# Kernel tuning notes

Measured on AMD Instinct MI355X. Metric: run time of the kernel, lower is better.

Reference implementation:

```python
import jax, jax.numpy as jnp
import numpy as np

B, N, H, NH, DEPTH = 4, 128, 512, 8, 4
HD = H // NH
TN = B * N
MH = int(H * 4.0)
EHD = 64
SCALE = HD ** -0.5

def _ln(x):
    m = jnp.mean(x, axis=-1, keepdims=True)
    v = jnp.mean(jnp.square(x - m), axis=-1, keepdims=True)
    return (x - m) * jax.lax.rsqrt(v + 1e-6)

def _gelu(x):
    return jax.nn.gelu(x, approximate=True)

def setup_inputs():
    rng = np.random.RandomState(0)
    topo_np = (rng.rand(B, N, N) < 0.15).astype(np.float32)
    sym = (topo_np + topo_np.transpose(0, 2, 1)) > 0
    b, i, j = np.nonzero(sym)  # same lexicographic order as torch nonzero
    edge_index = np.stack([i + b * N, j + b * N]).astype(np.int32)
    ks = jax.random.split(jax.random.key(0), 16)
    def w(k, shape, fan_in):
        return jax.random.normal(k, shape, jnp.float32) / np.float32(np.sqrt(fan_in))
    z = lambda *s: jnp.zeros(s, jnp.float32)
    return {
        "topo": jnp.asarray(topo_np),
        "weight": jax.random.normal(ks[0], (B, N), jnp.float32),
        "edge_index": jnp.asarray(edge_index),
        "w_topo": w(ks[1], (N, H), N), "b_topo": z(H),
        "w_w": w(ks[2], (1, H), 1), "b_w": z(H),
        "n_emb": 0.02 * jax.random.normal(ks[3], (N, H), jnp.float32),
        "wq": w(ks[4], (DEPTH, H, H), H), "bq": z(DEPTH, H),
        "wk": w(ks[5], (DEPTH, H, H), H), "bk": z(DEPTH, H),
        "wv": w(ks[6], (DEPTH, H, H), H), "bv": z(DEPTH, H),
        "wo": w(ks[7], (DEPTH, H, H), H), "bo": z(DEPTH, H),
        "w1": w(ks[8], (DEPTH, H, MH), H), "b1": z(DEPTH, MH),
        "w2": w(ks[9], (DEPTH, MH, H), MH), "b2": z(DEPTH, H),
        "ew1": w(ks[10], (3 * H, EHD), 3 * H), "eb1": z(EHD),
        "ew2": w(ks[11], (EHD, EHD), EHD), "eb2": z(EHD),
        "ew3": w(ks[12], (EHD, 1), EHD), "eb3": z(1),
    }

def _forward(topo, weight, edge_index, w_topo, b_topo, w_w, b_w, n_emb,
             wq, bq, wk, bk, wv, bv, wo, bo, w1, b1, w2, b2,
             ew1, eb1, ew2, eb2, ew3, eb3):
    src, dst = edge_index[0], edge_index[1]
    tsym = topo + jnp.swapaxes(topo, 1, 2)                      # (B,N,N)
    t = jnp.einsum('bnm,mh->bnh', tsym, w_topo) + b_topo        # topo_emb
    l = weight[..., None] * w_w[0] + b_w                        # weight_emb: Linear(1,H)
    x = (t + l + n_emb[None]).reshape(TN, H)
    for d in range(DEPTH):
        h = _ln(x)
        Q = (h @ wq[d] + bq[d]).reshape(TN, NH, HD)
        K = (h @ wk[d] + bk[d]).reshape(TN, NH, HD)
        V = (h @ wv[d] + bv[d]).reshape(TN, NH, HD)
        s = jnp.einsum('ehd,ehd->eh', Q[dst], K[src]) * SCALE   # (E,NH) per-edge QK dot
        m = jnp.maximum(jax.ops.segment_max(s, dst, num_segments=TN), -1e9)
        e = jnp.exp(s - m[dst])
        zs = jax.ops.segment_sum(e, dst, num_segments=TN)
        aw = e / (zs[dst] + 1e-12)                              # scatter_softmax
        msg = aw[..., None] * V[src]                            # (E,NH,HD)
        agg = jax.ops.segment_sum(msg, dst, num_segments=TN).reshape(TN, H)
        x = agg @ wo[d] + bo[d] + x
        h = _ln(x)
        x = _gelu(h @ w1[d] + b1[d]) @ w2[d] + b2[d] + x
    xb = x.reshape(B, N, H)
    xi = jnp.broadcast_to(xb[:, :, None, :], (B, N, N, H))
    xj = jnp.broadcast_to(xb[:, None, :, :], (B, N, N, H))
    f = jnp.concatenate([xi, xj, xi * xj], axis=-1)             # (B,N,N,3H)
    g = _gelu(f @ ew1 + eb1)
    g = _gelu(g @ ew2 + eb2)
    p = jax.nn.sigmoid((g @ ew3 + eb3)[..., 0])
    p = 0.5 * (p + jnp.swapaxes(p, 1, 2))
    p = p * (1.0 - jnp.eye(N, dtype=p.dtype))                   # zero diagonal
    p = p * (tsym > 0).astype(p.dtype)                          # mask to existing edges
    return p

def reference(topo, weight, edge_index, w_topo, b_topo, w_w, b_w, n_emb,
              wq, bq, wk, bk, wv, bv, wo, bo, w1, b1, w2, b2,
              ew1, eb1, ew2, eb2, ew3, eb3):
    return _forward(topo, weight, edge_index, w_topo, b_topo, w_w, b_w, n_emb,
                    wq, bq, wk, bk, wv, bv, wo, bo, w1, b1, w2, b2,
                    ew1, eb1, ew2, eb2, ew3, eb3)
```

## Files before the change

kernel.cpp:

```cpp
#include <hip/hip_runtime.h>
#include <hip/hip_bf16.h>
#include <math.h>

typedef __attribute__((ext_vector_type(8))) _Float16 f16x8;
typedef __attribute__((ext_vector_type(8))) short short8;
typedef __attribute__((ext_vector_type(4))) float f32x4;
typedef unsigned short u16;

__device__ __forceinline__ float gelu_f(float x) {
    float x3 = x * x * x;
    return 0.5f * x * (1.0f + tanhf(0.7978845608028654f * (x + 0.044715f * x3)));
}
__device__ __forceinline__ u16 f2h(float v) {
    _Float16 h = (_Float16)v;
    return *(u16*)&h;
}
__device__ __forceinline__ float h2f(u16 u) {
    _Float16 h = *(_Float16*)&u;
    return (float)h;
}

__global__ __launch_bounds__(256) void x0row_k(const float* __restrict__ topo,
                                               const float* __restrict__ weight,
                                               const float* __restrict__ w_topo,
                                               const float* __restrict__ b_topo,
                                               const float* __restrict__ w_w,
                                               const float* __restrict__ b_w,
                                               const float* __restrict__ n_emb,
                                               float* __restrict__ tsym,
                                               float* __restrict__ x,
                                               u16* __restrict__ h16) {
    int bn = blockIdx.x;
    int b = bn >> 7, n = bn & 127;
    int tid = threadIdx.x;
    __shared__ float tsr[128];
    __shared__ float red[256];
    if (tid < 128) {
        float v = topo[bn * 128 + tid] + topo[(b << 14) + (tid << 7) + n];
        tsr[tid] = v;
        tsym[bn * 128 + tid] = v;
    }
    __syncthreads();
    int c0 = tid, c1 = tid + 256;
    float acc0 = 0.f, acc1 = 0.f;
#pragma unroll 4
    for (int m = 0; m < 128; ++m) {
        float t = tsr[m];
        acc0 += t * w_topo[m * 512 + c0];
        acc1 += t * w_topo[m * 512 + c1];
    }
    float wgt = weight[bn];
    float v0 = acc0 + b_topo[c0] + wgt * w_w[c0] + b_w[c0] + n_emb[n * 512 + c0];
    float v1 = acc1 + b_topo[c1] + wgt * w_w[c1] + b_w[c1] + n_emb[n * 512 + c1];
    x[bn * 512 + c0] = v0;
    x[bn * 512 + c1] = v1;
    red[tid] = v0 + v1;
    __syncthreads();
    for (int off = 128; off > 0; off >>= 1) { if (tid < off) red[tid] += red[tid + off]; __syncthreads(); }
    float mean = red[0] * (1.0f / 512.0f);
    __syncthreads();
    float d0 = v0 - mean, d1 = v1 - mean;
    red[tid] = d0 * d0 + d1 * d1;
    __syncthreads();
    for (int off = 128; off > 0; off >>= 1) { if (tid < off) red[tid] += red[tid + off]; __syncthreads(); }
    float rs = rsqrtf(red[0] * (1.0f / 512.0f) + 1e-6f);
    h16[bn * 512 + c0] = f2h(d0 * rs);
    h16[bn * 512 + c1] = f2h(d1 * rs);
}

__global__ __launch_bounds__(256) void prep_k(
    const float* __restrict__ wq, const float* __restrict__ wk, const float* __restrict__ wv,
    const float* __restrict__ wo, const float* __restrict__ w1, const float* __restrict__ w2,
    const float* __restrict__ ew1,
    u16* __restrict__ qkvt, u16* __restrict__ wot,
    u16* __restrict__ w1t, u16* __restrict__ w2t,
    u16* __restrict__ eabt, u16* __restrict__ ect) {
    __shared__ u16 Hs[64][68];
    int bid = blockIdx.x;
    int region, tr, KK;
    u16* dh;
    if (bid < 768)       { region = 0; tr = bid;        KK = 512;  dh = qkvt; }
    else if (bid < 1024) { region = 1; tr = bid - 768;  KK = 512;  dh = wot; }
    else if (bid < 2048) { region = 2; tr = bid - 1024; KK = 512;  dh = w1t; }
    else if (bid < 3072) { region = 3; tr = bid - 2048; KK = 2048; dh = w2t; }
    else if (bid < 3088) { region = 4; tr = bid - 3072; KK = 512;  dh = eabt; }
    else                 { region = 5; tr = bid - 3088; KK = 512;  dh = ect; }
    int ktiles = KK >> 6;
    int tn = tr / ktiles, tk = tr % ktiles;
    int k0 = tk * 64, n0g = tn * 64;
    int tid = threadIdx.x;
#pragma unroll
    for (int p = 0; p < 4; ++p) {
        int kk = p * 16 + (tid >> 4);
        int nn = (tid & 15) * 4;
        int kg = k0 + kk, ng = n0g + nn;
        const float* src;
        if (region == 0) {
            int d = ng / 1536; int nr = ng - d * 1536; int sel = nr >> 9; int nc = nr & 511;
            const float* w = sel == 0 ? wq : (sel == 1 ? wk : wv);
            src = w + ((size_t)(d * 512 + kg)) * 512 + nc;
        } else if (region == 1) {
            int d = ng >> 9; int nc = ng & 511;
            src = wo + ((size_t)(d * 512 + kg)) * 512 + nc;
        } else if (region == 2) {
            int d = ng >> 11; int nc = ng & 2047;
            src = w1 + ((size_t)(d * 512 + kg)) * 2048 + nc;
        } else if (region == 3) {
            int d = ng >> 9; int nc = ng & 511;
            src = w2 + ((size_t)(d * 2048 + kg)) * 512 + nc;
        } else if (region == 4) {
            src = (ng < 64) ? (ew1 + (size_t)kg * 64 + ng) : (ew1 + (size_t)(512 + kg) * 64 + (ng - 64));
        } else {
            src = ew1 + (size_t)(1024 + kg) * 64 + ng;
        }
        float4 v = *(const float4*)src;
        *(ushort4*)&Hs[kk][nn] = make_ushort4(f2h(v.x), f2h(v.y), f2h(v.z), f2h(v.w));
    }
    __syncthreads();
#pragma unroll
    for (int p = 0; p < 2; ++p) {
        int chunk = p * 256 + tid;
        int nl = chunk >> 3;
        int k8 = (chunk & 7) * 8;
        ushort4 ha, hb;
        ha.x = Hs[k8 + 0][nl]; ha.y = Hs[k8 + 1][nl]; ha.z = Hs[k8 + 2][nl]; ha.w = Hs[k8 + 3][nl];
        hb.x = Hs[k8 + 4][nl]; hb.y = Hs[k8 + 5][nl]; hb.z = Hs[k8 + 6][nl]; hb.w = Hs[k8 + 7][nl];
        size_t dst = (size_t)(n0g + nl) * KK + k0 + k8;
        *(ushort4*)(dh + dst) = ha; *(ushort4*)(dh + dst + 4) = hb;
    }
}

template <int KC, bool PARTIAL, bool GELU, bool RES, bool OUTF, bool OUTS, bool EBIAS>
__global__ __launch_bounds__(256) void gemm2(
    const u16* __restrict__ A16, const u16* __restrict__ W16,
    const float* __restrict__ bias, const float* __restrict__ Rres,
    float* __restrict__ C, u16* __restrict__ C16,
    float* __restrict__ part, int lda, int N) {
    __shared__ u16 sbuf[2][2][64][32];
    const int tid = threadIdx.x;
    const int l = tid & 63;
    const int w = tid >> 6;
    const int bn0 = blockIdx.x * 64;
    const int bm0 = blockIdx.y * 64;
    const int z = blockIdx.z;

    const u16* gp[2];
#pragma unroll
    for (int i = 0; i < 2; ++i) {
        int o = (i * 4 + w) * 1024 + l * 16;
        int mat = o >> 12;
        int r = (o >> 6) & 63;
        int slot = (o >> 4) & 3;
        int lslot = slot ^ ((r >> 1) & 3);
        int kel = lslot * 8;
        const u16* basep = mat == 0 ? (A16 + (size_t)(bm0 + r) * lda)
                                    : (W16 + (size_t)(bn0 + r) * lda);
        gp[i] = basep + kel + z * KC;
    }

    f32x4 acc[2][2] = {};
    constexpr int S = KC / 32;

    auto stage = [&](int buf, int ko) {
#pragma unroll
        for (int i = 0; i < 2; ++i) {
            __builtin_amdgcn_global_load_lds(
                (const __attribute__((address_space(1))) void*)(gp[i] + ko),
                (__attribute__((address_space(3))) void*)((char*)&sbuf[buf][0][0][0] + (i * 4 + w) * 1024),
                16, 0, 0);
        }
    };
    auto compute = [&](int buf) {
        f16x8 a[2], b[2];
        int l15 = l & 15, lsl = l >> 4;
        int rA0 = (w & 1) * 32 + l15;
        int rB0 = (w >> 1) * 32 + l15;
#pragma unroll
        for (int f = 0; f < 2; ++f) {
            int rA = rA0 + f * 16;
            int rB = rB0 + f * 16;
            a[f] = *(const f16x8*)&sbuf[buf][0][rA][(lsl ^ ((rA >> 1) & 3)) * 8];
            b[f] = *(const f16x8*)&sbuf[buf][1][rB][(lsl ^ ((rB >> 1) & 3)) * 8];
        }
#pragma unroll
        for (int fm = 0; fm < 2; ++fm)
#pragma unroll
            for (int fn = 0; fn < 2; ++fn)
                acc[fm][fn] = __builtin_amdgcn_mfma_f32_16x16x32_f16(a[fm], b[fn], acc[fm][fn], 0, 0, 0);
    };

    stage(0, 0);
    __syncthreads();
#pragma unroll
    for (int s = 0; s < S; ++s) {
        if (s + 1 < S) stage((s + 1) & 1, (s + 1) * 32);
        compute(s & 1);
        __syncthreads();
    }

    int rb = bm0 + (w & 1) * 32 + ((l >> 4)) * 4;
    int cb = bn0 + (w >> 1) * 32 + (l & 15);
#pragma unroll
    for (int fm = 0; fm < 2; ++fm)
#pragma unroll
        for (int fn = 0; fn < 2; ++fn) {
            int col = cb + fn * 16;
            float bv;
            if (PARTIAL) bv = 0.f;
            else if (EBIAS) bv = col < 64 ? bias[col] : 0.f;
            else bv = bias[col];
#pragma unroll
            for (int r = 0; r < 4; ++r) {
                int row = rb + fm * 16 + r;
                float v = acc[fm][fn][r] + bv;
                if (PARTIAL) {
                    part[(size_t)z * 512 * N + (size_t)row * N + col] = v;
                } else {
                    if (GELU) v = gelu_f(v);
                    if (RES) v += Rres[(size_t)row * N + col];
                    if (OUTF) C[(size_t)row * N + col] = v;
                    if (OUTS) C16[(size_t)row * N + col] = f2h(v);
                }
            }
        }
}

template <int NZ, bool DOLN, bool DOSPLITX>
__global__ __launch_bounds__(256) void redln_k(const float* __restrict__ part,
                                               const float* __restrict__ bias,
                                               float* __restrict__ x,
                                               u16* __restrict__ h16) {
    int row = blockIdx.x;
    int tid = threadIdx.x;
    int c0 = tid, c1 = tid + 256;
    float v0 = bias[c0], v1 = bias[c1];
#pragma unroll
    for (int z = 0; z < NZ; ++z) {
        v0 += part[(size_t)z * 262144 + row * 512 + c0];
        v1 += part[(size_t)z * 262144 + row * 512 + c1];
    }
    v0 += x[row * 512 + c0];
    v1 += x[row * 512 + c1];
    x[row * 512 + c0] = v0;
    x[row * 512 + c1] = v1;
    if (DOSPLITX) {
        h16[row * 512 + c0] = f2h(v0);
        h16[row * 512 + c1] = f2h(v1);
    }
    if (DOLN) {
        __shared__ float red[256];
        red[tid] = v0 + v1;
        __syncthreads();
        for (int off = 128; off > 0; off >>= 1) { if (tid < off) red[tid] += red[tid + off]; __syncthreads(); }
        float mean = red[0] * (1.0f / 512.0f);
        __syncthreads();
        float d0 = v0 - mean, d1 = v1 - mean;
        red[tid] = d0 * d0 + d1 * d1;
        __syncthreads();
        for (int off = 128; off > 0; off >>= 1) { if (tid < off) red[tid] += red[tid + off]; __syncthreads(); }
        float rs = rsqrtf(red[0] * (1.0f / 512.0f) + 1e-6f);
        h16[row * 512 + c0] = f2h(d0 * rs);
        h16[row * 512 + c1] = f2h(d1 * rs);
    }
}

__global__ __launch_bounds__(256) void redqkv_k(const float* __restrict__ part,
                                                const float* __restrict__ bq,
                                                const float* __restrict__ bk,
                                                const float* __restrict__ bv,
                                                u16* __restrict__ qkv16) {
    int row = blockIdx.x;
    int tid = threadIdx.x;
#pragma unroll
    for (int u = 0; u < 6; ++u) {
        int col = tid + u * 256;
        float bias = col < 512 ? bq[col] : (col < 1024 ? bk[col - 512] : bv[col - 1024]);
        float v = bias + part[(size_t)row * 1536 + col]
                + part[(size_t)786432 + row * 1536 + col];
        qkv16[(size_t)row * 1536 + col] = f2h(v);
    }
}

__global__ __launch_bounds__(256) void attn_k(const u16* __restrict__ qkv16,
                                              const float* __restrict__ tsym,
                                              u16* __restrict__ agg16) {
    int tt = blockIdx.x, hh = blockIdx.y, b = blockIdx.z;
    __shared__ __align__(16) float Ks[128 * 68];
    __shared__ __align__(16) float Vt[64 * 132];
    __shared__ __align__(16) float Ss[16 * 132];
    __shared__ __align__(16) float Qs[16][68];
    int tid = threadIdx.x;
    {
        int j = tid >> 1, c0 = (tid & 1) * 32;
        const u16* kr = qkv16 + (size_t)(b * 128 + j) * 1536 + 512 + hh * 64 + c0;
        const u16* vr = kr + 512;
#pragma unroll
        for (int c = 0; c < 32; c += 8) {
            f16x8 kv = *(const f16x8*)(kr + c);
            f16x8 vv = *(const f16x8*)(vr + c);
#pragma unroll
            for (int q = 0; q < 8; ++q) {
                Ks[j * 68 + c0 + c + q] = (float)kv[q];
                Vt[(c0 + c + q) * 132 + j] = (float)vv[q];
            }
        }
    }
    {
        int rid = tid >> 4, c4 = (tid & 15) * 4;
        int grow = b * 128 + tt * 16 + rid;
        const u16* q0 = qkv16 + (size_t)grow * 1536 + hh * 64 + c4;
        Qs[rid][c4 + 0] = h2f(q0[0]);
        Qs[rid][c4 + 1] = h2f(q0[1]);
        Qs[rid][c4 + 2] = h2f(q0[2]);
        Qs[rid][c4 + 3] = h2f(q0[3]);
    }
    __syncthreads();
    {
        int j = tid & 127, th = tid >> 7;
        float acc[8] = {0.f, 0.f, 0.f, 0.f, 0.f, 0.f, 0.f, 0.f};
        for (int d0 = 0; d0 < 64; d0 += 4) {
            float4 kv = *(const float4*)&Ks[j * 68 + d0];
#pragma unroll
            for (int r = 0; r < 8; ++r) {
                float4 qv = *(const float4*)&Qs[th * 8 + r][d0];
                acc[r] += qv.x * kv.x + qv.y * kv.y + qv.z * kv.z + qv.w * kv.w;
            }
        }
        const float* tsr = tsym + ((size_t)b << 14) + (size_t)(tt * 16 + th * 8) * 128 + j;
#pragma unroll
        for (int r = 0; r < 8; ++r) {
            int t = th * 8 + r;
            float sv = (tsr[r * 128] > 0.f) ? acc[r] * 0.125f : -INFINITY;
            Ss[t * 132 + j] = sv;
        }
    }
    __syncthreads();
    {
        int row = tid >> 4, l16 = tid & 15;
        float v[8]; float m = -INFINITY;
#pragma unroll
        for (int c = 0; c < 8; ++c) { v[c] = Ss[row * 132 + l16 + c * 16]; m = fmaxf(m, v[c]); }
#pragma unroll
        for (int off = 8; off; off >>= 1) m = fmaxf(m, __shfl_xor(m, off));
        float ssum = 0.f;
#pragma unroll
        for (int c = 0; c < 8; ++c) {
            float e = (v[c] == -INFINITY) ? 0.f : __expf(v[c] - m);
            v[c] = e; ssum += e;
        }
#pragma unroll
        for (int off = 8; off; off >>= 1) ssum += __shfl_xor(ssum, off);
        float inv = 1.0f / (ssum + 1e-12f);
#pragma unroll
        for (int c = 0; c < 8; ++c) Ss[row * 132 + l16 + c * 16] = v[c] * inv;
    }
    __syncthreads();
    {
        int d = tid & 63, tq = tid >> 6;
        float a0 = 0.f, a1 = 0.f, a2 = 0.f, a3 = 0.f;
        for (int j0 = 0; j0 < 128; j0 += 4) {
            float4 vv = *(const float4*)&Vt[d * 132 + j0];
            float4 s0 = *(const float4*)&Ss[(tq * 4 + 0) * 132 + j0];
            float4 s1 = *(const float4*)&Ss[(tq * 4 + 1) * 132 + j0];
            float4 s2 = *(const float4*)&Ss[(tq * 4 + 2) * 132 + j0];
            float4 s3 = *(const float4*)&Ss[(tq * 4 + 3) * 132 + j0];
            a0 += s0.x * vv.x + s0.y * vv.y + s0.z * vv.z + s0.w * vv.w;
            a1 += s1.x * vv.x + s1.y * vv.y + s1.z * vv.z + s1.w * vv.w;
            a2 += s2.x * vv.x + s2.y * vv.y + s2.z * vv.z + s2.w * vv.w;
            a3 += s3.x * vv.x + s3.y * vv.y + s3.z * vv.z + s3.w * vv.w;
        }
        float accv[4] = {a0, a1, a2, a3};
        int growbase = b * 128 + tt * 16;
#pragma unroll
        for (int i = 0; i < 4; ++i) {
            int t = tq * 4 + i;
            agg16[(size_t)(growbase + t) * 512 + hh * 64 + d] = f2h(accv[i]);
        }
    }
}

__global__ __launch_bounds__(256) void redae_k(const float* __restrict__ part,
                                               const float* __restrict__ eb1,
                                               float* __restrict__ aebe) {
    int idx = blockIdx.x * 256 + threadIdx.x;
    int col = idx & 127;
    float v = col < 64 ? eb1[col] : 0.0f;
#pragma unroll
    for (int z = 0; z < 4; ++z) v += part[(size_t)z * 65536 + idx];
    aebe[idx] = v;
}

__global__ __launch_bounds__(256) void cross_k(const float* __restrict__ x,
                                               const u16* __restrict__ ect,
                                               float* __restrict__ C3) {
    int i = blockIdx.x, b = blockIdx.y;
    __shared__ float xis[512];
    __shared__ u16 As[2][128][32];
    int tid = threadIdx.x;
    {
        const float* xip = x + (size_t)(b * 128 + i) * 512;
        xis[tid] = xip[tid];
        xis[tid + 256] = xip[tid + 256];
    }
    int r = tid >> 1, half = tid & 1, koff = half * 16;
    const float* xr = x + (size_t)(b * 128 + r) * 512 + koff;
    int sw_r = (r >> 1) & 3;
    int lane = tid & 63, w = tid >> 6;
    int m0 = (w & 1) * 64, n0 = (w >> 1) * 32;
    int l15 = lane & 15, lsl = lane >> 4, kf = lsl * 8;
    const u16* pB0 = ect + (size_t)(n0 + l15) * 512 + kf;
    const u16* pB1 = ect + (size_t)(n0 + 16 + l15) * 512 + kf;
    f32x4 acc[4][2] = {};

    auto stageA = [&](int buf, int kbase) {
        float4 v0 = *(const float4*)(xr + kbase);
        float4 v1 = *(const float4*)(xr + kbase + 4);
        float4 v2 = *(const float4*)(xr + kbase + 8);
        float4 v3 = *(const float4*)(xr + kbase + 12);
        float xv[16] = {v0.x, v0.y, v0.z, v0.w, v1.x, v1.y, v1.z, v1.w,
                        v2.x, v2.y, v2.z, v2.w, v3.x, v3.y, v3.z, v3.w};
        short8 h0, h1;
#pragma unroll
        for (int q = 0; q < 8; ++q)
            h0[q] = (short)f2h(xv[q] * xis[kbase + koff + q]);
#pragma unroll
        for (int q = 0; q < 8; ++q)
            h1[q] = (short)f2h(xv[8 + q] * xis[kbase + koff + 8 + q]);
        *(short8*)&As[buf][r][((2 * half + 0) ^ sw_r) * 8] = h0;
        *(short8*)&As[buf][r][((2 * half + 1) ^ sw_r) * 8] = h1;
    };
    auto computeC = [&](int buf, int kbase) {
        f16x8 b0 = *(const f16x8*)(pB0 + kbase);
        f16x8 b1 = *(const f16x8*)(pB1 + kbase);
#pragma unroll
        for (int mf = 0; mf < 4; ++mf) {
            int rA = m0 + mf * 16 + l15;
            f16x8 ah = *(const f16x8*)&As[buf][rA][(lsl ^ ((rA >> 1) & 3)) * 8];
            acc[mf][0] = __builtin_amdgcn_mfma_f32_16x16x32_f16(ah, b0, acc[mf][0], 0, 0, 0);
            acc[mf][1] = __builtin_amdgcn_mfma_f32_16x16x32_f16(ah, b1, acc[mf][1], 0, 0, 0);
        }
    };

    __syncthreads();
    stageA(0, 0);
    __syncthreads();
    for (int s = 0; s < 16; ++s) {
        if (s < 15) stageA((s + 1) & 1, (s + 1) * 32);
        computeC(s & 1, s * 32);
        __syncthreads();
    }

    float* outp = C3 + (size_t)(b * 128 + i) * 128 * 64;
#pragma unroll
    for (int mf = 0; mf < 4; ++mf)
#pragma unroll
        for (int nf = 0; nf < 2; ++nf)
#pragma unroll
            for (int q = 0; q < 4; ++q)
                outp[(size_t)(m0 + mf * 16 + lsl * 4 + q) * 64 + (n0 + nf * 16 + l15)] = acc[mf][nf][q];
}

__global__ __launch_bounds__(256) void efin_k(const int* __restrict__ ei, int E,
                                              const float* __restrict__ C3,
                                              const float* __restrict__ aebe,
                                              const float* __restrict__ ew2, const float* __restrict__ eb2,
                                              const float* __restrict__ ew3, const float* __restrict__ eb3,
                                              float* __restrict__ P) {
    __shared__ float G1[32][66];
    __shared__ float G2[32][66];
    __shared__ int s_src[32], s_dst[32];
    int tid = threadIdx.x;
    int e0 = blockIdx.x * 32;
    if (tid < 32) {
        int e = e0 + tid;
        s_src[tid] = e < E ? ei[e] : 0;
        s_dst[tid] = e < E ? ei[E + e] : 0;
    }
    __syncthreads();
    {
        int e = tid >> 3, c8 = (tid & 7) * 8;
        int s = s_src[e], d = s_dst[e];
        int bB = s >> 7, i2 = s & 127, j2 = d & 127;
        const float* c3 = C3 + ((size_t)(bB * 128 + i2) * 128 + j2) * 64 + c8;
        const float* ap = aebe + (size_t)s * 128 + c8;
        const float* bp = aebe + (size_t)d * 128 + 64 + c8;
#pragma unroll
        for (int q = 0; q < 8; ++q)
            G1[e][c8 + q] = gelu_f(c3[q] + ap[q] + bp[q]);
    }
    __syncthreads();
    {
        int col = tid & 63, eq = tid >> 6;
        float acc[8];
#pragma unroll
        for (int i = 0; i < 8; ++i) acc[i] = eb2[col];
        for (int m = 0; m < 64; ++m) {
            float wv = ew2[m * 64 + col];
#pragma unroll
            for (int i = 0; i < 8; ++i) acc[i] += G1[eq * 8 + i][m] * wv;
        }
#pragma unroll
        for (int i = 0; i < 8; ++i) G2[eq * 8 + i][col] = gelu_f(acc[i]);
    }
    __syncthreads();
    {
        int el2 = tid >> 3, c8 = (tid & 7) * 8;
        float p = 0.f;
#pragma unroll
        for (int i = 0; i < 8; ++i) p += G2[el2][c8 + i] * ew3[c8 + i];
        p += __shfl_xor(p, 1); p += __shfl_xor(p, 2); p += __shfl_xor(p, 4);
        if ((tid & 7) == 0 && e0 + el2 < E) {
            float logit = p + eb3[0];
            int s = s_src[el2], d2 = s_dst[el2];
            int bB = s >> 7, i2 = s & 127, j2 = d2 & 127;
            P[(bB << 14) + (i2 << 7) + j2] = 1.0f / (1.0f + expf(-logit));
        }
    }
}

__global__ __launch_bounds__(256) void final_k(const float* __restrict__ tsym,
                                               const float* __restrict__ P,
                                               float* __restrict__ out) {
    int idx = blockIdx.x * 256 + threadIdx.x;
    int b = idx >> 14, i = (idx >> 7) & 127, j = idx & 127;
    float o = 0.0f;
    if (i != j && tsym[idx] > 0.0f)
        o = 0.5f * (P[idx] + P[(b << 14) + (j << 7) + i]);
    out[idx] = o;
}

extern "C" void kernel_launch(void* const* d_in, const int* in_sizes, int n_in,
                              void* d_out, int out_size, void* d_ws, size_t ws_size,
                              hipStream_t stream) {
    const float* topo   = (const float*)d_in[0];
    const float* weight = (const float*)d_in[1];
    const int*   ei     = (const int*)d_in[2];
    const float* w_topo = (const float*)d_in[3];
    const float* b_topo = (const float*)d_in[4];
    const float* w_w    = (const float*)d_in[5];
    const float* b_w    = (const float*)d_in[6];
    const float* n_emb  = (const float*)d_in[7];
    const float* wq = (const float*)d_in[8];  const float* bq = (const float*)d_in[9];
    const float* wk = (const float*)d_in[10]; const float* bk = (const float*)d_in[11];
    const float* wv = (const float*)d_in[12]; const float* bv = (const float*)d_in[13];
    const float* wo = (const float*)d_in[14]; const float* bo = (const float*)d_in[15];
    const float* w1 = (const float*)d_in[16]; const float* b1 = (const float*)d_in[17];
    const float* w2 = (const float*)d_in[18]; const float* b2 = (const float*)d_in[19];
    const float* ew1 = (const float*)d_in[20]; const float* eb1 = (const float*)d_in[21];
    const float* ew2 = (const float*)d_in[22]; const float* eb2 = (const float*)d_in[23];
    const float* ew3 = (const float*)d_in[24]; const float* eb3 = (const float*)d_in[25];
    const int E = in_sizes[2] / 2;

    char* base = (char*)d_ws;
    size_t off = 0;
    auto alloc = [&](size_t bytes) { char* p = base + off; off += (bytes + 255) & ~(size_t)255; return p; };
    u16* qkvt = (u16*)alloc(3145728 * 2);
    u16* wot  = (u16*)alloc(1048576 * 2);
    u16* w1t  = (u16*)alloc(4194304 * 2);
    u16* w2t  = (u16*)alloc(4194304 * 2);
    u16* eabt = (u16*)alloc(65536 * 2);
    u16* ect  = (u16*)alloc(32768 * 2);
    u16* h16   = (u16*)alloc(262144 * 2);
    u16* agg16 = (u16*)alloc(262144 * 2);
    u16* mid16 = (u16*)alloc(1048576 * 2);
    u16* x16   = (u16*)alloc(262144 * 2);
    u16* qkv16 = (u16*)alloc(786432 * 2);
    float* tsym  = (float*)alloc(65536 * 4);
    float* x     = (float*)alloc(262144 * 4);
    float* aebe  = (float*)alloc(65536 * 4);
    float* P     = (float*)alloc(65536 * 4);
    float* pw    = (float*)alloc(1572864 * 4);
    float* C3    = (float*)alloc((size_t)16777216 * 4);

    prep_k<<<3096, 256, 0, stream>>>(wq, wk, wv, wo, w1, w2, ew1,
                                     qkvt, wot, w1t, w2t, eabt, ect);
    x0row_k<<<512, 256, 0, stream>>>(topo, weight, w_topo, b_topo, w_w, b_w, n_emb,
                                     tsym, x, h16);

    for (int d = 0; d < 4; ++d) {
        gemm2<256, true, false, false, false, false, false><<<dim3(24, 8, 2), 256, 0, stream>>>(
            h16, qkvt + (size_t)d * 1536 * 512,
            nullptr, nullptr, nullptr, nullptr, pw, 512, 1536);
        redqkv_k<<<512, 256, 0, stream>>>(pw, bq + d * 512, bk + d * 512, bv + d * 512, qkv16);
        attn_k<<<dim3(8, 8, 4), 256, 0, stream>>>(qkv16, tsym, agg16);
        gemm2<128, true, false, false, false, false, false><<<dim3(8, 8, 4), 256, 0, stream>>>(
            agg16, wot + (size_t)d * 512 * 512,
            nullptr, nullptr, nullptr, nullptr, pw, 512, 512);
        redln_k<4, true, false><<<512, 256, 0, stream>>>(pw, bo + d * 512, x, h16);
        gemm2<512, false, true, false, false, true, false><<<dim3(32, 8, 1), 256, 0, stream>>>(
            h16, w1t + (size_t)d * 2048 * 512,
            b1 + d * 2048, nullptr, nullptr, mid16, nullptr, 512, 2048);
        gemm2<512, true, false, false, false, false, false><<<dim3(8, 8, 4), 256, 0, stream>>>(
            mid16, w2t + (size_t)d * 512 * 2048,
            nullptr, nullptr, nullptr, nullptr, pw, 2048, 512);
        if (d < 3) {
            redln_k<4, true, false><<<512, 256, 0, stream>>>(pw, b2 + d * 512, x, h16);
        } else {
            redln_k<4, false, true><<<512, 256, 0, stream>>>(pw, b2 + d * 512, x, x16);
        }
    }

    gemm2<128, true, false, false, false, false, false><<<dim3(2, 8, 4), 256, 0, stream>>>(
        x16, eabt, nullptr, nullptr, nullptr, nullptr, pw, 512, 128);
    redae_k<<<256, 256, 0, stream>>>(pw, eb1, aebe);
    cross_k<<<dim3(128, 4), 256, 0, stream>>>(x, ect, C3);
    efin_k<<<(E + 31) / 32, 256, 0, stream>>>(ei, E, C3, aebe, ew2, eb2, ew3, eb3, P);
    final_k<<<256, 256, 0, stream>>>(tsym, P, (float*)d_out);
}
```

Measured before the change: 256.9 us.

## Store pairwise edge intermediate in fp16 and fold x0 init into weight prep

The large per-pair cross-term buffer C3 (B*N*N*64 elements) is now written by cross_k as fp16 instead of fp32 and read in efin_k with a single 8-wide vector load, halving the traffic of that intermediate. Separately, the initial embedding plus layernorm kernel is merged into the weight-prep kernel as an extra 512 blocks, removing one launch. The fp16 storage adds rounding error to the edge MLP input before GELU.

```diff
diff --git a/kernel.cpp b/kernel.cpp
--- a/kernel.cpp
+++ b/kernel.cpp
@@ -18,54 +18,6 @@
 __device__ __forceinline__ float h2f(u16 u) {
     _Float16 h = *(_Float16*)&u;
     return (float)h;
-}
-
-__global__ __launch_bounds__(256) void x0row_k(const float* __restrict__ topo,
-                                               const float* __restrict__ weight,
-                                               const float* __restrict__ w_topo,
-                                               const float* __restrict__ b_topo,
-                                               const float* __restrict__ w_w,
-                                               const float* __restrict__ b_w,
-                                               const float* __restrict__ n_emb,
-                                               float* __restrict__ tsym,
-                                               float* __restrict__ x,
-                                               u16* __restrict__ h16) {
-    int bn = blockIdx.x;
-    int b = bn >> 7, n = bn & 127;
-    int tid = threadIdx.x;
-    __shared__ float tsr[128];
-    __shared__ float red[256];
-    if (tid < 128) {
-        float v = topo[bn * 128 + tid] + topo[(b << 14) + (tid << 7) + n];
-        tsr[tid] = v;
-        tsym[bn * 128 + tid] = v;
-    }
-    __syncthreads();
-    int c0 = tid, c1 = tid + 256;
-    float acc0 = 0.f, acc1 = 0.f;
-#pragma unroll 4
-    for (int m = 0; m < 128; ++m) {
-        float t = tsr[m];
-        acc0 += t * w_topo[m * 512 + c0];
-        acc1 += t * w_topo[m * 512 + c1];
-    }
-    float wgt = weight[bn];
-    float v0 = acc0 + b_topo[c0] + wgt * w_w[c0] + b_w[c0] + n_emb[n * 512 + c0];
-    float v1 = acc1 + b_topo[c1] + wgt * w_w[c1] + b_w[c1] + n_emb[n * 512 + c1];
-    x[bn * 512 + c0] = v0;
-    x[bn * 512 + c1] = v1;
-    red[tid] = v0 + v1;
-    __syncthreads();
-    for (int off = 128; off > 0; off >>= 1) { if (tid < off) red[tid] += red[tid + off]; __syncthreads(); }
-    float mean = red[0] * (1.0f / 512.0f);
-    __syncthreads();
-    float d0 = v0 - mean, d1 = v1 - mean;
-    red[tid] = d0 * d0 + d1 * d1;
-    __syncthreads();
-    for (int off = 128; off > 0; off >>= 1) { if (tid < off) red[tid] += red[tid + off]; __syncthreads(); }
-    float rs = rsqrtf(red[0] * (1.0f / 512.0f) + 1e-6f);
-    h16[bn * 512 + c0] = f2h(d0 * rs);
-    h16[bn * 512 + c1] = f2h(d1 * rs);
 }
 
 __global__ __launch_bounds__(256) void prep_k(
@@ -74,9 +26,55 @@
     const float* __restrict__ ew1,
     u16* __restrict__ qkvt, u16* __restrict__ wot,
     u16* __restrict__ w1t, u16* __restrict__ w2t,
-    u16* __restrict__ eabt, u16* __restrict__ ect) {
+    u16* __restrict__ eabt, u16* __restrict__ ect,
+    const float* __restrict__ topo, const float* __restrict__ weight,
+    const float* __restrict__ w_topo, const float* __restrict__ b_topo,
+    const float* __restrict__ w_w, const float* __restrict__ b_w,
+    const float* __restrict__ n_emb,
+    float* __restrict__ tsym, float* __restrict__ x, u16* __restrict__ h16) {
     __shared__ u16 Hs[64][68];
+    __shared__ float tsr[128];
+    __shared__ float red[256];
     int bid = blockIdx.x;
+    int tid = threadIdx.x;
+
+    if (bid >= 3096) {
+        int bn = bid - 3096;
+        int b = bn >> 7, n = bn & 127;
+        if (tid < 128) {
+            float v = topo[bn * 128 + tid] + topo[(b << 14) + (tid << 7) + n];
+            tsr[tid] = v;
+            tsym[bn * 128 + tid] = v;
+        }
+        __syncthreads();
+        int c0 = tid, c1 = tid + 256;
+        float acc0 = 0.f, acc1 = 0.f;
+#pragma unroll 4
+        for (int m = 0; m < 128; ++m) {
+            float t = tsr[m];
+            acc0 += t * w_topo[m * 512 + c0];
+            acc1 += t * w_topo[m * 512 + c1];
+        }
+        float wgt = weight[bn];
+        float v0 = acc0 + b_topo[c0] + wgt * w_w[c0] + b_w[c0] + n_emb[n * 512 + c0];
+        float v1 = acc1 + b_topo[c1] + wgt * w_w[c1] + b_w[c1] + n_emb[n * 512 + c1];
+        x[bn * 512 + c0] = v0;
+        x[bn * 512 + c1] = v1;
+        red[tid] = v0 + v1;
+        __syncthreads();
+        for (int off = 128; off > 0; off >>= 1) { if (tid < off) red[tid] += red[tid + off]; __syncthreads(); }
+        float mean = red[0] * (1.0f / 512.0f);
+        __syncthreads();
+        float d0 = v0 - mean, d1 = v1 - mean;
+        red[tid] = d0 * d0 + d1 * d1;
+        __syncthreads();
+        for (int off = 128; off > 0; off >>= 1) { if (tid < off) red[tid] += red[tid + off]; __syncthreads(); }
+        float rs = rsqrtf(red[0] * (1.0f / 512.0f) + 1e-6f);
+        h16[bn * 512 + c0] = f2h(d0 * rs);
+        h16[bn * 512 + c1] = f2h(d1 * rs);
+        return;
+    }
+
     int region, tr, KK;
     u16* dh;
     if (bid < 768)       { region = 0; tr = bid;        KK = 512;  dh = qkvt; }
@@ -88,7 +86,6 @@
     int ktiles = KK >> 6;
     int tn = tr / ktiles, tk = tr % ktiles;
     int k0 = tk * 64, n0g = tn * 64;
-    int tid = threadIdx.x;
 #pragma unroll
     for (int p = 0; p < 4; ++p) {
         int kk = p * 16 + (tid >> 4);
@@ -392,7 +389,7 @@
 
 __global__ __launch_bounds__(256) void cross_k(const float* __restrict__ x,
                                                const u16* __restrict__ ect,
-                                               float* __restrict__ C3) {
+                                               u16* __restrict__ C3) {
     int i = blockIdx.x, b = blockIdx.y;
     __shared__ float xis[512];
     __shared__ u16 As[2][128][32];
@@ -450,18 +447,19 @@
         __syncthreads();
     }
 
-    float* outp = C3 + (size_t)(b * 128 + i) * 128 * 64;
+    u16* outp = C3 + (size_t)(b * 128 + i) * 128 * 64;
 #pragma unroll
     for (int mf = 0; mf < 4; ++mf)
 #pragma unroll
         for (int nf = 0; nf < 2; ++nf)
 #pragma unroll
             for (int q = 0; q < 4; ++q)
-                outp[(size_t)(m0 + mf * 16 + lsl * 4 + q) * 64 + (n0 + nf * 16 + l15)] = acc[mf][nf][q];
+                outp[(size_t)(m0 + mf * 16 + lsl * 4 + q) * 64 + (n0 + nf * 16 + l15)] =
+                    f2h(acc[mf][nf][q]);
 }
 
 __global__ __launch_bounds__(256) void efin_k(const int* __restrict__ ei, int E,
-                                              const float* __restrict__ C3,
+                                              const u16* __restrict__ C3,
                                               const float* __restrict__ aebe,
                                               const float* __restrict__ ew2, const float* __restrict__ eb2,
                                               const float* __restrict__ ew3, const float* __restrict__ eb3,
@@ -481,12 +479,13 @@
         int e = tid >> 3, c8 = (tid & 7) * 8;
         int s = s_src[e], d = s_dst[e];
         int bB = s >> 7, i2 = s & 127, j2 = d & 127;
-        const float* c3 = C3 + ((size_t)(bB * 128 + i2) * 128 + j2) * 64 + c8;
+        const u16* c3 = C3 + ((size_t)(bB * 128 + i2) * 128 + j2) * 64 + c8;
         const float* ap = aebe + (size_t)s * 128 + c8;
         const float* bp = aebe + (size_t)d * 128 + 64 + c8;
+        f16x8 cv = *(const f16x8*)c3;
 #pragma unroll
         for (int q = 0; q < 8; ++q)
-            G1[e][c8 + q] = gelu_f(c3[q] + ap[q] + bp[q]);
+            G1[e][c8 + q] = gelu_f((float)cv[q] + ap[q] + bp[q]);
     }
     __syncthreads();
     {
@@ -565,16 +564,16 @@
     u16* mid16 = (u16*)alloc(1048576 * 2);
     u16* x16   = (u16*)alloc(262144 * 2);
     u16* qkv16 = (u16*)alloc(786432 * 2);
+    u16* C3    = (u16*)alloc((size_t)16777216 * 2);
     float* tsym  = (float*)alloc(65536 * 4);
     float* x     = (float*)alloc(262144 * 4);
     float* aebe  = (float*)alloc(65536 * 4);
     float* P     = (float*)alloc(65536 * 4);
     float* pw    = (float*)alloc(1572864 * 4);
-    float* C3    = (float*)alloc((size_t)16777216 * 4);
-
-    prep_k<<<3096, 256, 0, stream>>>(wq, wk, wv, wo, w1, w2, ew1,
-                                     qkvt, wot, w1t, w2t, eabt, ect);
-    x0row_k<<<512, 256, 0, stream>>>(topo, weight, w_topo, b_topo, w_w, b_w, n_emb,
+
+    prep_k<<<3608, 256, 0, stream>>>(wq, wk, wv, wo, w1, w2, ew1,
+                                     qkvt, wot, w1t, w2t, eabt, ect,
+                                     topo, weight, w_topo, b_topo, w_w, b_w, n_emb,
                                      tsym, x, h16);
 
     for (int d = 0; d < 4; ++d) {
```

Result: faster. 248.4 us (-3.3%).
